# Kernel optimization log

Measured on AMD Instinct MI355X. Metric: run time of the kernel, lower is better.

## Reference

```python
import jax, jax.numpy as jnp
import numpy as np
import math

DIM = 1024

def setup_inputs() -> dict:
    key = jax.random.key(0)
    ks = jax.random.split(key, 5)
    X = jax.random.normal(ks[0], (4, 2048, DIM), dtype=jnp.float32)
    # Linear params (stored as [in, out] so y = x @ W + b)
    W_in = jax.random.normal(ks[1], (DIM, 3 * DIM), dtype=jnp.float32) / math.sqrt(DIM)
    b_in = jnp.zeros((3 * DIM,), dtype=jnp.float32)
    W_out = jax.random.normal(ks[2], (DIM, DIM), dtype=jnp.float32) / math.sqrt(DIM)
    b_out = jnp.zeros((DIM,), dtype=jnp.float32)
    return {"X": X, "W_in": W_in, "b_in": b_in, "W_out": W_out, "b_out": b_out}

def reference(X, W_in, b_in, W_out, b_out):
    dim = X.shape[-1]
    QKV = X @ W_in + b_in                       # [B, S, 3*dim]
    Q, K, V = jnp.split(QKV, 3, axis=-1)        # each [B, S, dim]
    scores = jnp.einsum('bqd,bkd->bqk', Q, K) / math.sqrt(dim)  # [B, S, S]
    attn = jax.nn.softmax(scores, axis=-1)
    out = jnp.einsum('bqk,bkd->bqd', attn, V)   # [B, S, dim]
    return out @ W_out + b_out
```

## Files before the change

### kernel.cpp

```cpp
#include <hip/hip_runtime.h>
#include <hip/hip_bf16.h>
#include <math.h>

typedef __attribute__((ext_vector_type(8))) __bf16 bf16x8;
typedef __attribute__((ext_vector_type(4))) float f32x4;

#define DIM 1024
#define SEQ 2048
#define BATCH 4
#define ROWS (BATCH*SEQ)

#define BAR() do { asm volatile("" ::: "memory"); __builtin_amdgcn_s_barrier(); asm volatile("" ::: "memory"); } while(0)
#define WAITV(n) asm volatile("s_waitcnt vmcnt(" #n ")" ::: "memory")

__device__ __forceinline__ unsigned short f2bf(float f) {
  unsigned int u = __float_as_uint(f);
  u += 0x7FFF + ((u >> 16) & 1);
  return (unsigned short)(u >> 16);
}
__device__ __forceinline__ unsigned short to_bf_bits(float v) { return f2bf(v); }
__device__ __forceinline__ unsigned short to_bf_bits(unsigned short v) { return v; }

__device__ __forceinline__ void gload_lds16(const void* g, void* lds) {
  __builtin_amdgcn_global_load_lds((__attribute__((address_space(1))) void*)g,
                                   (__attribute__((address_space(3))) void*)lds,
                                   16, 0, 0);
}

__global__ __launch_bounds__(256)
void conv_f32_bf16(const float* __restrict__ src, unsigned short* __restrict__ dst, int n8) {
  int i = blockIdx.x * blockDim.x + threadIdx.x;
  if (i >= n8) return;
  const float4* s = reinterpret_cast<const float4*>(src) + (size_t)i * 2;
  float4 a = s[0], b = s[1];
  union { unsigned short h[8]; uint4 v; } p;
  p.h[0]=f2bf(a.x); p.h[1]=f2bf(a.y); p.h[2]=f2bf(a.z); p.h[3]=f2bf(a.w);
  p.h[4]=f2bf(b.x); p.h[5]=f2bf(b.y); p.h[6]=f2bf(b.z); p.h[7]=f2bf(b.w);
  reinterpret_cast<uint4*>(dst)[i] = p.v;
}

template<typename Tin>
__global__ __launch_bounds__(1024)
void transpose_conv(const Tin* __restrict__ src, int ldsrc, size_t sstride,
                    unsigned short* __restrict__ dst, int lddst, size_t dstride) {
  __shared__ unsigned short tile[32][33];
  const Tin* s = src + (size_t)blockIdx.z * sstride;
  unsigned short* d = dst + (size_t)blockIdx.z * dstride;
  int tx = threadIdx.x, ty = threadIdx.y;
  int r = blockIdx.y * 32 + ty, c = blockIdx.x * 32 + tx;
  tile[ty][tx] = to_bf_bits(s[(size_t)r * ldsrc + c]);
  __syncthreads();
  d[(size_t)(blockIdx.x * 32 + ty) * lddst + blockIdx.y * 32 + tx] = tile[tx][ty];
}

#define EPI_QKV 0
#define EPI_F32 1
#define EPI_BF16 2
#define EPI_BIAS_F32 3

template<int BN, int EPI>
__global__ __launch_bounds__(512, 2)
void gemm8(const unsigned short* __restrict__ A, int lda, size_t sA,
           const unsigned short* __restrict__ B, int ldb, size_t sB,
           void* __restrict__ C, int ldc, size_t sC,
           const float* __restrict__ bias, int K) {
  constexpr int NREP = BN / 64;
  constexpr int NW = 16 * NREP;
  constexpr int BCH = BN / 16;
  __shared__ unsigned short As[4 * 256 * 32];
  __shared__ unsigned short Bs[4 * BN * 32];

  const int tid = threadIdx.x;
  const int lane = tid & 63, wave = tid >> 6;
  const int wm = wave >> 2, wn = wave & 3;
  const int fr = lane & 15, fk = lane >> 4;
  const int tileM = blockIdx.y * 256, tileN = blockIdx.x * BN;
  const unsigned short* Ab = A + (size_t)blockIdx.z * sA;
  const unsigned short* Bb = B + (size_t)blockIdx.z * sB;
  const int srow = lane >> 2;
  const int sslot = lane & 3;

  auto stage = [&](int sl, int k0) {
#pragma unroll
    for (int q = 0; q < 2; ++q) {
      int c = wave + q * 8;
      int r = c * 16 + srow;
      int g = sslot ^ ((r >> 1) & 3);
      gload_lds16(Ab + (size_t)(tileM + r) * lda + k0 + g * 8,
                  &As[sl * (256 * 32) + c * 512]);
    }
#pragma unroll
    for (int q = 0; q < BCH / 8; ++q) {
      int c = wave + q * 8;
      int r = c * 16 + srow;
      int g = sslot ^ ((r >> 1) & 3);
      gload_lds16(Bb + (size_t)(tileN + r) * ldb + k0 + g * 8,
                  &Bs[sl * (BN * 32) + c * 512]);
    }
  };

  f32x4 acc[8][NREP];
#pragma unroll
  for (int m = 0; m < 8; ++m)
#pragma unroll
    for (int n = 0; n < NREP; ++n) acc[m][n] = (f32x4){0.f, 0.f, 0.f, 0.f};

  const int NS = K >> 5;
  stage(0, 0);
  stage(1, 32);

  for (int p = 0; p < NS; ++p) {
    if (p + 2 < NS) {
      stage((p + 2) & 3, (p + 2) << 5);
      if (BN == 256) { WAITV(8); } else { WAITV(6); }
    } else if (p + 2 == NS) {
      if (BN == 256) { WAITV(4); } else { WAITV(3); }
    } else {
      WAITV(0);
    }
    BAR();
    const unsigned short* Asl = &As[(p & 3) * (256 * 32)];
    const unsigned short* Bsl = &Bs[(p & 3) * (BN * 32)];
    bf16x8 af[8], bg[NREP];
#pragma unroll
    for (int m = 0; m < 8; ++m) {
      int r = wm * 128 + m * 16 + fr;
      af[m] = *reinterpret_cast<const bf16x8*>(&Asl[r * 32 + ((fk ^ ((r >> 1) & 3)) * 8)]);
    }
#pragma unroll
    for (int n = 0; n < NREP; ++n) {
      int r = wn * NW + n * 16 + fr;
      bg[n] = *reinterpret_cast<const bf16x8*>(&Bsl[r * 32 + ((fk ^ ((r >> 1) & 3)) * 8)]);
    }
    __builtin_amdgcn_s_setprio(1);
#pragma unroll
    for (int m = 0; m < 8; ++m)
#pragma unroll
      for (int n = 0; n < NREP; ++n)
        acc[m][n] = __builtin_amdgcn_mfma_f32_16x16x32_bf16(af[m], bg[n], acc[m][n], 0, 0, 0);
    __builtin_amdgcn_s_setprio(0);
  }

#pragma unroll
  for (int m = 0; m < 8; ++m)
#pragma unroll
    for (int n = 0; n < NREP; ++n)
#pragma unroll
      for (int j = 0; j < 4; ++j) {
        int row = tileM + wm * 128 + m * 16 + fk * 4 + j;
        int col = tileN + wn * NW + n * 16 + fr;
        float v = acc[m][n][j];
        if (EPI == EPI_QKV) {
          v += bias[col];
          if (col < DIM) v *= 0.03125f;
          ((unsigned short*)C + (size_t)blockIdx.z * sC)[(size_t)row * ldc + col] = f2bf(v);
        } else if (EPI == EPI_BF16) {
          ((unsigned short*)C + (size_t)blockIdx.z * sC)[(size_t)row * ldc + col] = f2bf(v);
        } else if (EPI == EPI_BIAS_F32) {
          ((float*)C + (size_t)blockIdx.z * sC)[(size_t)row * ldc + col] = v + bias[col];
        } else {
          ((float*)C + (size_t)blockIdx.z * sC)[(size_t)row * ldc + col] = v;
        }
      }
}

__global__ __launch_bounds__(256)
void softmax_kernel(float* __restrict__ S, size_t zstride) {
  __shared__ float red[8];
  float* row = S + (size_t)blockIdx.y * zstride + (size_t)blockIdx.x * SEQ;
  const int tid = threadIdx.x;
  const int lane = tid & 63, wave = tid >> 6;
  const float4* src = reinterpret_cast<const float4*>(row) + tid * 2;
  float4 a = src[0], b = src[1];
  float v[8] = {a.x, a.y, a.z, a.w, b.x, b.y, b.z, b.w};
  float m = v[0];
#pragma unroll
  for (int i = 1; i < 8; ++i) m = fmaxf(m, v[i]);
  for (int o = 32; o; o >>= 1) m = fmaxf(m, __shfl_xor(m, o));
  if (lane == 0) red[wave] = m;
  __syncthreads();
  m = fmaxf(fmaxf(red[0], red[1]), fmaxf(red[2], red[3]));
  float e[8], s = 0.f;
#pragma unroll
  for (int i = 0; i < 8; ++i) { e[i] = expf(v[i] - m); s += e[i]; }
  for (int o = 32; o; o >>= 1) s += __shfl_xor(s, o);
  if (lane == 0) red[4 + wave] = s;
  __syncthreads();
  s = red[4] + red[5] + red[6] + red[7];
  float inv = 1.f / s;
  union { unsigned short h[8]; uint4 u; } p;
#pragma unroll
  for (int i = 0; i < 8; ++i) p.h[i] = f2bf(e[i] * inv);
  reinterpret_cast<uint4*>(row)[tid] = p.u;
}

extern "C" void kernel_launch(void* const* d_in, const int* in_sizes, int n_in,
                              void* d_out, int out_size, void* d_ws, size_t ws_size,
                              hipStream_t stream) {
  const float* X     = (const float*)d_in[0];
  const float* W_in  = (const float*)d_in[1];
  const float* b_in  = (const float*)d_in[2];
  const float* W_out = (const float*)d_in[3];
  const float* b_out = (const float*)d_in[4];
  float* out = (float*)d_out;
  char* ws = (char*)d_ws;

  size_t o = 0;
  auto alloc = [&](size_t bytes) { size_t r = o; o += (bytes + 255) & ~(size_t)255; return r; };
  unsigned short* Xbf   = (unsigned short*)(ws + alloc((size_t)ROWS * DIM * 2));
  unsigned short* WinT  = (unsigned short*)(ws + alloc((size_t)3 * DIM * DIM * 2));
  unsigned short* WoutT = (unsigned short*)(ws + alloc((size_t)DIM * DIM * 2));
  unsigned short* QKV   = (unsigned short*)(ws + alloc((size_t)ROWS * 3 * DIM * 2));
  size_t fixed = o;
  size_t per_batch = (((size_t)SEQ * SEQ * 4 + 255) & ~(size_t)255) +
                     (((size_t)DIM * SEQ * 2 + 255) & ~(size_t)255);
  int G = (ws_size >= fixed + 4 * per_batch) ? BATCH : 1;
  float*          Sc = (float*)(ws + alloc((size_t)G * SEQ * SEQ * 4));
  unsigned short* Vt = (unsigned short*)(ws + alloc((size_t)G * DIM * SEQ * 2));
  unsigned short* O  = Xbf;

  conv_f32_bf16<<<(ROWS * DIM / 8 + 255) / 256, 256, 0, stream>>>(X, Xbf, ROWS * DIM / 8);
  transpose_conv<float><<<dim3(3 * DIM / 32, DIM / 32, 1), dim3(32, 32), 0, stream>>>(
      W_in, 3 * DIM, 0, WinT, DIM, 0);
  transpose_conv<float><<<dim3(DIM / 32, DIM / 32, 1), dim3(32, 32), 0, stream>>>(
      W_out, DIM, 0, WoutT, DIM, 0);
  gemm8<256, EPI_QKV><<<dim3(3 * DIM / 256, ROWS / 256, 1), 512, 0, stream>>>(
      Xbf, DIM, 0, WinT, DIM, 0, QKV, 3 * DIM, 0, b_in, DIM);

  for (int b0 = 0; b0 < BATCH; b0 += G) {
    const unsigned short* Qb = QKV + (size_t)b0 * SEQ * 3 * DIM;
    const unsigned short* Kb = Qb + DIM;
    const unsigned short* Vb = Qb + 2 * DIM;
    transpose_conv<unsigned short><<<dim3(DIM / 32, SEQ / 32, G), dim3(32, 32), 0, stream>>>(
        Vb, 3 * DIM, (size_t)SEQ * 3 * DIM, Vt, SEQ, (size_t)DIM * SEQ);
    gemm8<256, EPI_F32><<<dim3(SEQ / 256, SEQ / 256, G), 512, 0, stream>>>(
        Qb, 3 * DIM, (size_t)SEQ * 3 * DIM, Kb, 3 * DIM, (size_t)SEQ * 3 * DIM,
        Sc, SEQ, (size_t)SEQ * SEQ, nullptr, DIM);
    softmax_kernel<<<dim3(SEQ, G), 256, 0, stream>>>(Sc, (size_t)SEQ * SEQ);
    gemm8<128, EPI_BF16><<<dim3(DIM / 128, SEQ / 256, G), 512, 0, stream>>>(
        (const unsigned short*)Sc, 2 * SEQ, (size_t)2 * SEQ * SEQ,
        Vt, SEQ, (size_t)DIM * SEQ,
        O + (size_t)b0 * SEQ * DIM, DIM, (size_t)SEQ * DIM, nullptr, SEQ);
  }
  gemm8<128, EPI_BIAS_F32><<<dim3(DIM / 128, ROWS / 256, 1), 512, 0, stream>>>(
      O, DIM, 0, WoutT, DIM, 0, out, DIM, 0, b_out, DIM);
}
```

Baseline: 243.8 us.

## Restructure GEMM mainloop into K=64 double-buffered four-quadrant ping-pong schedule

The bf16 MFMA GEMM moves from a 4-slot ring of K=32 stages to two K=64 LDS buffers with an 8-way XOR swizzle. Each iteration is split into four MFMA quadrants (lo/hi M × lo/hi N). Fragment reads from LDS and partial global-to-LDS loads for the next tile are interleaved between the quadrants, fenced by barriers and sched_barrier. The aim is finer-grained overlap of memory and MFMA work, with half as many waitcnt/barrier rounds per unit of K. In exchange it adds many more barriers per iteration and more register pressure from holding fragments for both halves.

```diff
diff --git a/kernel.cpp b/kernel.cpp
--- a/kernel.cpp
+++ b/kernel.cpp
@@ -12,6 +12,7 @@
 
 #define BAR() do { asm volatile("" ::: "memory"); __builtin_amdgcn_s_barrier(); asm volatile("" ::: "memory"); } while(0)
 #define WAITV(n) asm volatile("s_waitcnt vmcnt(" #n ")" ::: "memory")
+#define SCHED0() __builtin_amdgcn_sched_barrier(0)
 
 __device__ __forceinline__ unsigned short f2bf(float f) {
   unsigned int u = __float_as_uint(f);
@@ -53,6 +54,19 @@
   d[(size_t)(blockIdx.x * 32 + ty) * lddst + blockIdx.y * 32 + tx] = tile[tx][ty];
 }
 
+template<int NREP, int NLO, int MB, int NBASE>
+__device__ __forceinline__ void quad(f32x4 (&acc)[8][NREP], const bf16x8 (&af)[4][2],
+                                     const bf16x8 (&bg)[NLO][2]) {
+#pragma unroll
+  for (int kk = 0; kk < 2; ++kk)
+#pragma unroll
+    for (int m = 0; m < 4; ++m)
+#pragma unroll
+      for (int n = 0; n < NLO; ++n)
+        acc[MB + m][NBASE + n] =
+            __builtin_amdgcn_mfma_f32_16x16x32_bf16(af[m][kk], bg[n][kk], acc[MB + m][NBASE + n], 0, 0, 0);
+}
+
 #define EPI_QKV 0
 #define EPI_F32 1
 #define EPI_BF16 2
@@ -65,10 +79,10 @@
            void* __restrict__ C, int ldc, size_t sC,
            const float* __restrict__ bias, int K) {
   constexpr int NREP = BN / 64;
+  constexpr int NLO = NREP / 2;
   constexpr int NW = 16 * NREP;
-  constexpr int BCH = BN / 16;
-  __shared__ unsigned short As[4 * 256 * 32];
-  __shared__ unsigned short Bs[4 * BN * 32];
+  __shared__ unsigned short As[2 * 256 * 64];
+  __shared__ unsigned short Bs[2 * BN * 64];
 
   const int tid = threadIdx.x;
   const int lane = tid & 63, wave = tid >> 6;
@@ -77,27 +91,26 @@
   const int tileM = blockIdx.y * 256, tileN = blockIdx.x * BN;
   const unsigned short* Ab = A + (size_t)blockIdx.z * sA;
   const unsigned short* Bb = B + (size_t)blockIdx.z * sB;
-  const int srow = lane >> 2;
-  const int sslot = lane & 3;
-
-  auto stage = [&](int sl, int k0) {
+
+  const int srow = tid >> 3;
+  const int sg = (tid & 7) ^ (srow & 7);
+
+  auto stageA = [&](int buf, int half, int k0) {
 #pragma unroll
     for (int q = 0; q < 2; ++q) {
-      int c = wave + q * 8;
-      int r = c * 16 + srow;
-      int g = sslot ^ ((r >> 1) & 3);
-      gload_lds16(Ab + (size_t)(tileM + r) * lda + k0 + g * 8,
-                  &As[sl * (256 * 32) + c * 512]);
-    }
-#pragma unroll
-    for (int q = 0; q < BCH / 8; ++q) {
-      int c = wave + q * 8;
-      int r = c * 16 + srow;
-      int g = sslot ^ ((r >> 1) & 3);
-      gload_lds16(Bb + (size_t)(tileN + r) * ldb + k0 + g * 8,
-                  &Bs[sl * (BN * 32) + c * 512]);
+      int rl = half * 128 + q * 64 + srow;
+      gload_lds16(Ab + (size_t)(tileM + rl) * lda + k0 + sg * 8,
+                  &As[buf * (256 * 64) + (half * 128 + q * 64) * 64 + tid * 8]);
     }
   };
+  auto stageB = [&](int buf, int part, int k0) {
+#pragma unroll
+    for (int q = 0; q < 2; ++q) {
+      int rl = part * 128 + q * 64 + srow;
+      gload_lds16(Bb + (size_t)(tileN + rl) * ldb + k0 + sg * 8,
+                  &Bs[buf * (BN * 64) + (part * 128 + q * 64) * 64 + tid * 8]);
+    }
+  };
 
   f32x4 acc[8][NREP];
 #pragma unroll
@@ -105,40 +118,76 @@
 #pragma unroll
     for (int n = 0; n < NREP; ++n) acc[m][n] = (f32x4){0.f, 0.f, 0.f, 0.f};
 
-  const int NS = K >> 5;
-  stage(0, 0);
-  stage(1, 32);
-
-  for (int p = 0; p < NS; ++p) {
-    if (p + 2 < NS) {
-      stage((p + 2) & 3, (p + 2) << 5);
-      if (BN == 256) { WAITV(8); } else { WAITV(6); }
-    } else if (p + 2 == NS) {
-      if (BN == 256) { WAITV(4); } else { WAITV(3); }
-    } else {
-      WAITV(0);
-    }
-    BAR();
-    const unsigned short* Asl = &As[(p & 3) * (256 * 32)];
-    const unsigned short* Bsl = &Bs[(p & 3) * (BN * 32)];
-    bf16x8 af[8], bg[NREP];
-#pragma unroll
-    for (int m = 0; m < 8; ++m) {
-      int r = wm * 128 + m * 16 + fr;
-      af[m] = *reinterpret_cast<const bf16x8*>(&Asl[r * 32 + ((fk ^ ((r >> 1) & 3)) * 8)]);
-    }
-#pragma unroll
-    for (int n = 0; n < NREP; ++n) {
-      int r = wn * NW + n * 16 + fr;
-      bg[n] = *reinterpret_cast<const bf16x8*>(&Bsl[r * 32 + ((fk ^ ((r >> 1) & 3)) * 8)]);
-    }
-    __builtin_amdgcn_s_setprio(1);
-#pragma unroll
-    for (int m = 0; m < 8; ++m)
-#pragma unroll
-      for (int n = 0; n < NREP; ++n)
-        acc[m][n] = __builtin_amdgcn_mfma_f32_16x16x32_bf16(af[m], bg[n], acc[m][n], 0, 0, 0);
-    __builtin_amdgcn_s_setprio(0);
+  const int NS = K >> 6;
+  stageA(0, 0, 0); stageA(0, 1, 0); stageB(0, 0, 0);
+  if (BN == 256) stageB(0, 1, 0);
+  stageA(1, 0, 64);
+
+  bf16x8 afLo[4][2], afHi[4][2], bgLo[NLO][2], bgHi[NLO][2];
+
+  for (int t = 0; t < NS; ++t) {
+    const int cb = t & 1, nb = cb ^ 1;
+    const unsigned short* Asl = &As[cb * (256 * 64)];
+    const unsigned short* Bsl = &Bs[cb * (BN * 64)];
+    const int k1 = (t + 1) << 6, k2 = (t + 2) << 6;
+
+    if (t + 1 < NS) { WAITV(2); } else { WAITV(0); }
+    BAR();
+#pragma unroll
+    for (int m = 0; m < 4; ++m) {
+      int rl = wm * 128 + m * 16 + fr;
+#pragma unroll
+      for (int kk = 0; kk < 2; ++kk)
+        afLo[m][kk] = *(const bf16x8*)&Asl[rl * 64 + (((kk * 4 + fk) ^ (rl & 7)) << 3)];
+    }
+#pragma unroll
+    for (int n = 0; n < NLO; ++n) {
+      int rl = wn * NW + n * 16 + fr;
+#pragma unroll
+      for (int kk = 0; kk < 2; ++kk)
+        bgLo[n][kk] = *(const bf16x8*)&Bsl[rl * 64 + (((kk * 4 + fk) ^ (rl & 7)) << 3)];
+    }
+    if (t + 1 < NS) stageA(nb, 1, k1);
+    BAR(); SCHED0();
+    __builtin_amdgcn_s_setprio(1);
+    quad<NREP, NLO, 0, 0>(acc, afLo, bgLo);
+    __builtin_amdgcn_s_setprio(0); SCHED0();
+    BAR();
+
+#pragma unroll
+    for (int n = 0; n < NLO; ++n) {
+      int rl = wn * NW + (NLO + n) * 16 + fr;
+#pragma unroll
+      for (int kk = 0; kk < 2; ++kk)
+        bgHi[n][kk] = *(const bf16x8*)&Bsl[rl * 64 + (((kk * 4 + fk) ^ (rl & 7)) << 3)];
+    }
+    if (t + 1 < NS) stageB(nb, 0, k1);
+    BAR(); SCHED0();
+    __builtin_amdgcn_s_setprio(1);
+    quad<NREP, NLO, 0, NLO>(acc, afLo, bgHi);
+    __builtin_amdgcn_s_setprio(0); SCHED0();
+    BAR();
+
+#pragma unroll
+    for (int m = 0; m < 4; ++m) {
+      int rl = wm * 128 + (4 + m) * 16 + fr;
+#pragma unroll
+      for (int kk = 0; kk < 2; ++kk)
+        afHi[m][kk] = *(const bf16x8*)&Asl[rl * 64 + (((kk * 4 + fk) ^ (rl & 7)) << 3)];
+    }
+    if (BN == 256) { if (t + 1 < NS) stageB(nb, 1, k1); }
+    BAR(); SCHED0();
+    __builtin_amdgcn_s_setprio(1);
+    quad<NREP, NLO, 4, 0>(acc, afHi, bgLo);
+    __builtin_amdgcn_s_setprio(0); SCHED0();
+    BAR();
+
+    if (t + 2 < NS) stageA(cb, 0, k2);
+    BAR(); SCHED0();
+    __builtin_amdgcn_s_setprio(1);
+    quad<NREP, NLO, 4, NLO>(acc, afHi, bgHi);
+    __builtin_amdgcn_s_setprio(0); SCHED0();
+    BAR();
   }
 
 #pragma unroll
```

Result: no change. 244.5 us (+0.3%).
